# Kernel optimization log

Hardware: AMD Instinct MI355X
Metric: run time of the kernel (lower is better)

Reference implementation:

```python
import jax, jax.numpy as jnp
import numpy as np
from jax.scipy.special import digamma, gammaln

NUM_CLASSES = 3
FOCAL_GAMMA = 2.0
LABEL_SMOOTHING = 0.1
EVIDENTIAL_W = 0.1
CONTRASTIVE_W = 0.1
BOUNDARY_W = 0.15
TRIPLET_W = 0.1
QUALITY_W = 0.1
TRIPLET_MARGIN = 1.5


def setup_inputs() -> dict:
    key = jax.random.key(0)
    k1, k2, k3 = jax.random.split(key, 3)
    B, D = 4096, 512
    logits = jax.random.normal(k1, (B, NUM_CLASSES), dtype=jnp.float32)
    targets = jax.random.randint(k2, (B,), 0, 3)
    features = jax.random.normal(k3, (B, D), dtype=jnp.float32)
    alpha = jax.random.uniform(jax.random.fold_in(key, 7), (B, NUM_CLASSES), dtype=jnp.float32)
    focal_alpha = jnp.array([1.0, 2.0, 1.5], dtype=jnp.float32)
    class_weights = jnp.array([1.0, 2.0, 1.5], dtype=jnp.float32)
    return {"logits": logits, "targets": targets, "features": features,
            "alpha": alpha, "epoch": 1, "focal_alpha": focal_alpha,
            "class_weights": class_weights}


def reference(logits, targets, features, alpha, epoch, focal_alpha, class_weights):
    B = logits.shape[0]
    C = NUM_CLASSES

    # ---- focal loss (label-smoothed CE, torch semantics) ----
    logp = jax.nn.log_softmax(logits, axis=1)                      # [B,C]
    nll = -jnp.take_along_axis(logp, targets[:, None], axis=1)[:, 0]
    ce_ls = (1.0 - LABEL_SMOOTHING) * nll + LABEL_SMOOTHING * (-logp.mean(axis=1))
    pt = jnp.exp(-ce_ls)
    focal = (focal_alpha[targets] * (1.0 - pt) ** FOCAL_GAMMA * ce_ls).mean()

    # ---- weighted CE (torch weighted mean: sum(w*nll)/sum(w)) ----
    w = class_weights[targets]
    ce = (w * nll).sum() / w.sum()

    # ---- enhanced boundary loss ----
    probs = jax.nn.softmax(logits, axis=1)
    real = targets == 0
    semi = targets == 1
    syn = targets == 2
    rb = jnp.where(real, probs[:, 1] + 0.6 * probs[:, 2], 0.0).sum()
    sb = jnp.where(syn, probs[:, 1] + 0.4 * probs[:, 0], 0.0).sum()
    mb = jnp.where(semi, 1.0 - probs[:, 1] + 0.3 * (probs[:, 0] + probs[:, 2]), 0.0).sum()
    boundary = (rb + sb + 4.5 * mb) / (B + 1e-8)

    total = 0.4 * focal + 0.3 * ce + BOUNDARY_W * boundary

    # ---- normalized features and pairwise cosine-sim matrix ----
    norms = jnp.linalg.norm(features, axis=1, keepdims=True)
    f = features / jnp.maximum(norms, 1e-12)
    sim = f @ f.T                                                  # [B,B]
    same = targets[:, None] == targets[None, :]
    eye = jnp.eye(B, dtype=bool)

    # ---- enhanced contrastive loss ----
    pos = jnp.where(same, (1.0 - sim) ** 2, 0.0).sum()
    neg = jnp.where(~same, jnp.clip(sim - 0.2, 0.0) ** 2, 0.0).sum()
    semi_pair = semi[:, None] & semi[None, :]
    semi_l = jnp.where(semi_pair, (1.0 - sim) ** 2, 0.0).sum()
    contrastive = (pos + neg + 4.0 * semi_l) / (B * B + 1e-8)

    # ---- enhanced triplet loss (batch-hard, vectorized) ----
    d2 = jnp.clip(2.0 - 2.0 * sim, 0.0)
    dist = jnp.sqrt(jnp.where(eye, 1.0, d2))  # diag masked; safe sqrt
    pos_mask = same & ~eye
    neg_mask = ~same
    hp = jnp.max(jnp.where(pos_mask, dist, -jnp.inf), axis=1)
    hn = jnp.min(jnp.where(neg_mask, dist, jnp.inf), axis=1)
    valid = pos_mask.any(axis=1) & neg_mask.any(axis=1)
    margin = TRIPLET_MARGIN * jnp.where(targets == 1, 2.5, 1.0)
    tl = jax.nn.relu(hp - hn + margin)
    cnt = valid.sum()
    triplet = jnp.where(cnt > 0,
                        jnp.where(valid, tl, 0.0).sum() / jnp.maximum(cnt, 1),
                        0.0)

    # ---- quality-invariant loss (upper-tri same-class pairs) ----
    upper = jnp.triu(jnp.ones((B, B), dtype=bool), k=1)
    qmask = same & upper
    npairs = qmask.sum()
    q = jnp.where(qmask, (1.0 - sim) ** 2, 0.0).sum() / jnp.maximum(npairs, 1)
    frac2 = syn.astype(jnp.float32).mean()
    q = q * jnp.where(syn.sum() > 0, 1.0 + 2.5 * frac2, 1.0)
    quality = jnp.where(npairs > 0, q, 0.0)

    # ---- evidential loss ----
    onehot = jax.nn.one_hot(targets, C, dtype=jnp.float32)
    S = alpha.sum(axis=1, keepdims=True) + 1e-8
    likelihood = (onehot * (digamma(S) - digamma(alpha + 1e-8))).sum(axis=1)
    at = onehot + (1.0 - onehot) * alpha
    ats = at.sum(axis=1) + 1e-8
    kl = (gammaln(ats) - gammaln(at + 1e-8).sum(axis=1)
          + ((at - 1.0) * (digamma(at + 1e-8) - digamma(ats[:, None] + 1e-8))).sum(axis=1))
    annealing = min(1.0, (epoch / 25.0) ** 2)
    evidential = likelihood.mean() + annealing * 0.2 * kl.mean()

    total = (total + CONTRASTIVE_W * contrastive + TRIPLET_W * triplet
             + QUALITY_W * quality + EVIDENTIAL_W * evidential)
    return total
```

## Files before the change

kernel.cpp:

```cpp
#include <hip/hip_runtime.h>
#include <hip/hip_bf16.h>
#include <cstdint>

typedef __attribute__((ext_vector_type(8))) __bf16 bf8;
typedef __attribute__((ext_vector_type(4))) float f32x4;

#if defined(__has_builtin)
#if __has_builtin(__builtin_amdgcn_global_load_lds)
#define USE_GLL 1
#endif
#endif
#ifndef USE_GLL
#define USE_GLL 0
#endif

#if USE_GLL
__device__ __forceinline__ void gll16(const __bf16* g, __bf16* l){
  __builtin_amdgcn_global_load_lds(
      (const __attribute__((address_space(1))) void*)g,
      (__attribute__((address_space(3))) void*)l, 16, 0, 0);
}
#endif

__device__ __forceinline__ unsigned mapf(float x){
  unsigned u = __float_as_uint(x);
  return (u & 0x80000000u) ? ~u : (u | 0x80000000u);
}
__device__ __forceinline__ float unmapf(unsigned u){
  return __uint_as_float((u & 0x80000000u) ? (u & 0x7FFFFFFFu) : ~u);
}

__device__ float digammaf_(float x){
  float r = 0.f;
  while (x < 6.f){ r -= 1.f/x; x += 1.f; }
  float inv = 1.f/x, inv2 = inv*inv;
  r += logf(x) - 0.5f*inv
     - inv2*(0.08333333333f - inv2*(0.008333333333f - inv2*0.003968253968f));
  return r;
}

__global__ __launch_bounds__(256) void k_prep(const float* __restrict__ feat,
    __bf16* __restrict__ fb,
    const float* __restrict__ logits, const int* __restrict__ targets,
    const float* __restrict__ alpha,  const float* __restrict__ fa,
    const float* __restrict__ cw, int B, int D,
    float* __restrict__ psum, unsigned* __restrict__ pcnt,
    float* __restrict__ acc, unsigned* rowMinU, unsigned* rowMaxU){
  int bid = blockIdx.x, tid = threadIdx.x;
  int wave = tid >> 6, lane = tid & 63;

  int row = bid*4 + wave;
  if (row < B){
    const float* src = feat + (size_t)row*D;
    float ss = 0.f;
    for (int c = lane*4; c < D; c += 64*4){
      float4 v = *(const float4*)(src + c);
      ss += v.x*v.x + v.y*v.y + v.z*v.z + v.w*v.w;
    }
    #pragma unroll
    for (int off=32; off; off>>=1) ss += __shfl_xor(ss, off);
    float inv = 1.f / fmaxf(sqrtf(ss), 1e-12f);
    __bf16* dst = fb + (size_t)row*D;
    for (int c = lane*8; c < D; c += 64*8){
      float4 v0 = *(const float4*)(src + c);
      float4 v1 = *(const float4*)(src + c + 4);
      bf8 o;
      o[0]=(__bf16)(v0.x*inv); o[1]=(__bf16)(v0.y*inv);
      o[2]=(__bf16)(v0.z*inv); o[3]=(__bf16)(v0.w*inv);
      o[4]=(__bf16)(v1.x*inv); o[5]=(__bf16)(v1.y*inv);
      o[6]=(__bf16)(v1.z*inv); o[7]=(__bf16)(v1.w*inv);
      *(bf8*)(dst + c) = o;
    }
  }

  int SB = B >> 8;
  if (bid == SB && tid < 16) acc[tid] = 0.f;
  if (bid >= SB) return;

  int i = bid*256 + tid;
  rowMinU[i] = 0xFFFFFFFFu; rowMaxU[i] = 0u;

  float l0=logits[3*i], l1=logits[3*i+1], l2=logits[3*i+2];
  int t = targets[i];
  float m = fmaxf(l0, fmaxf(l1,l2));
  float e0=expf(l0-m), e1=expf(l1-m), e2=expf(l2-m);
  float se = e0+e1+e2;
  float lse = m + logf(se);
  float lp0=l0-lse, lp1=l1-lse, lp2=l2-lse;
  float lpt = (t==0)?lp0:((t==1)?lp1:lp2);
  float nll = -lpt;
  float ce_ls = 0.9f*nll + 0.1f*(-(lp0+lp1+lp2)*(1.f/3.f));
  float pt = expf(-ce_ls);
  float om = 1.f - pt;
  float focal_i = fa[t]*om*om*ce_ls;
  float w = cw[t];
  float ce_n = w*nll, ce_d = w;
  float p0=e0/se, p1=e1/se, p2=e2/se;
  float bnd;
  if (t==0)      bnd = p1 + 0.6f*p2;
  else if (t==2) bnd = p1 + 0.4f*p0;
  else           bnd = 4.5f*(1.f - p1 + 0.3f*(p0+p2));
  float a0=alpha[3*i], a1=alpha[3*i+1], a2=alpha[3*i+2];
  float S = a0+a1+a2 + 1e-8f;
  float at_ = (t==0)?a0:((t==1)?a1:a2);
  float lik = digammaf_(S) - digammaf_(at_ + 1e-8f);
  float b0 = (t==0)?1.f:a0, b1 = (t==1)?1.f:a1, b2 = (t==2)?1.f:a2;
  float ats = b0+b1+b2 + 1e-8f;
  float psa = digammaf_(ats + 1e-8f);
  float kl = lgammaf(ats)
     - (lgammaf(b0+1e-8f)+lgammaf(b1+1e-8f)+lgammaf(b2+1e-8f))
     + (b0-1.f)*(digammaf_(b0+1e-8f)-psa)
     + (b1-1.f)*(digammaf_(b1+1e-8f)-psa)
     + (b2-1.f)*(digammaf_(b2+1e-8f)-psa);

  unsigned long long m0 = __ballot(t==0);
  unsigned long long m1 = __ballot(t==1);
  unsigned long long m2 = __ballot(t==2);
  #pragma unroll
  for (int off=32; off; off>>=1){
    focal_i += __shfl_xor(focal_i, off);
    ce_n    += __shfl_xor(ce_n, off);
    ce_d    += __shfl_xor(ce_d, off);
    bnd     += __shfl_xor(bnd, off);
    lik     += __shfl_xor(lik, off);
    kl      += __shfl_xor(kl, off);
  }
  if (lane == 0){
    int slot = bid*4 + wave;
    psum[slot*8+0]=focal_i; psum[slot*8+1]=ce_n; psum[slot*8+2]=ce_d;
    psum[slot*8+3]=bnd;     psum[slot*8+4]=lik;  psum[slot*8+5]=kl;
    pcnt[slot*4+0]=(unsigned)__popcll(m0);
    pcnt[slot*4+1]=(unsigned)__popcll(m1);
    pcnt[slot*4+2]=(unsigned)__popcll(m2);
  }
}

__global__ __launch_bounds__(256) void k_pairs(const __bf16* __restrict__ fb,
    const int* __restrict__ targets, int B, int D,
    float* acc, unsigned* rowMinU, unsigned* rowMaxU){
  __shared__ __bf16 sA[2][4096];
  __shared__ __bf16 sB[2][4096];
  __shared__ int sRT[128];
  __shared__ int sCT[128];
  __shared__ float sred[4][4];

  int t = blockIdx.x;
  int bx = (int)((sqrtf(8.f*(float)t + 1.f) - 1.f)*0.5f);
  while ((bx+1)*(bx+2)/2 <= t) bx++;
  while (bx*(bx+1)/2 > t) bx--;
  int by = t - bx*(bx+1)/2;
  bool isDiag = (by == bx);
  int rowBase = by*128, colBase = bx*128;

  int tid = threadIdx.x, lane = tid & 63, wave = tid >> 6;
  int wr = wave >> 1, wc = wave & 1;
  int quad = lane >> 4, l16 = lane & 15;

  if (tid < 128) sRT[tid] = targets[rowBase + tid];
  else           sCT[tid-128] = targets[colBase + tid - 128];

  const __bf16* gA[2]; const __bf16* gB[2];
  #pragma unroll
  for (int r=0; r<2; r++){
    int e = tid*8 + r*2048;
    int row = e >> 5;
    int cb = (e & 31) >> 3;
    int gcb = cb ^ ((row >> 1) & 3);
    gA[r] = fb + (size_t)(rowBase + row)*D + gcb*8;
    gB[r] = fb + (size_t)(colBase + row)*D + gcb*8;
  }
  int wofs = wave*512;

  int offA[4], offB[4];
  #pragma unroll
  for (int mi=0; mi<4; mi++){
    int R = wr*64 + mi*16 + l16;
    offA[mi] = R*32 + ((quad ^ ((R>>1)&3))*8);
  }
  #pragma unroll
  for (int ni=0; ni<4; ni++){
    int R = wc*64 + ni*16 + l16;
    offB[ni] = R*32 + ((quad ^ ((R>>1)&3))*8);
  }

#if USE_GLL
  #pragma unroll
  for (int r=0; r<2; r++){
    gll16(gA[r], &sA[0][wofs + r*2048]);
    gll16(gB[r], &sB[0][wofs + r*2048]);
  }
#else
  #pragma unroll
  for (int r=0; r<2; r++){
    *(bf8*)&sA[0][tid*8 + r*2048] = *(const bf8*)gA[r];
    *(bf8*)&sB[0][tid*8 + r*2048] = *(const bf8*)gB[r];
  }
#endif

  f32x4 C[4][4] = {};
  int NIT = D/32;
  int cur = 0;

  for (int it=0; it<NIT; ++it){
    __syncthreads();
    if (it+1 < NIT){
      int k0 = (it+1)*32;
      int nb = cur ^ 1;
#if USE_GLL
      #pragma unroll
      for (int r=0; r<2; r++){
        gll16(gA[r]+k0, &sA[nb][wofs + r*2048]);
        gll16(gB[r]+k0, &sB[nb][wofs + r*2048]);
      }
#else
      #pragma unroll
      for (int r=0; r<2; r++){
        *(bf8*)&sA[nb][tid*8 + r*2048] = *(const bf8*)(gA[r]+k0);
        *(bf8*)&sB[nb][tid*8 + r*2048] = *(const bf8*)(gB[r]+k0);
      }
#endif
    }
    bf8 aF[4], bF[4];
    #pragma unroll
    for (int mi=0; mi<4; mi++) aF[mi] = *(const bf8*)(&sA[cur][offA[mi]]);
    #pragma unroll
    for (int ni=0; ni<4; ni++) bF[ni] = *(const bf8*)(&sB[cur][offB[ni]]);
    #pragma unroll
    for (int mi=0; mi<4; mi++)
      #pragma unroll
      for (int ni=0; ni<4; ni++)
        C[mi][ni] = __builtin_amdgcn_mfma_f32_16x16x32_bf16(aF[mi], bF[ni], C[mi][ni], 0,0,0);
    cur ^= 1;
  }

  int tcol[4];
  #pragma unroll
  for (int ni=0; ni<4; ni++) tcol[ni] = sCT[wc*64 + ni*16 + l16];

  float pos=0.f, neg=0.f, semi=0.f, diag=0.f;
  float cmin[4], cmax[4];
  #pragma unroll
  for (int ni=0; ni<4; ni++){ cmin[ni]=2.f; cmax[ni]=-2.f; }

  #pragma unroll
  for (int mi=0; mi<4; mi++){
    #pragma unroll
    for (int r=0; r<4; r++){
      int rl = wr*64 + mi*16 + quad*4 + r;
      int row = rowBase + rl;
      int tr = sRT[rl];
      float vmin = 2.f, vmax = -2.f;
      #pragma unroll
      for (int ni=0; ni<4; ni++){
        int col = colBase + wc*64 + ni*16 + l16;
        float s = C[mi][ni][r];
        if (tr == tcol[ni]){
          float omv = 1.f - s;
          float q = omv*omv;
          pos += q;
          if (tr == 1) semi += q;
          if (row == col) diag += q;
          else {
            vmin = fminf(vmin, s);
            cmin[ni] = fminf(cmin[ni], s);
          }
        } else {
          float c0 = fmaxf(s - 0.2f, 0.f);
          neg += c0*c0;
          vmax = fmaxf(vmax, s);
          cmax[ni] = fmaxf(cmax[ni], s);
        }
      }
      #pragma unroll
      for (int off=1; off<16; off<<=1){
        vmin = fminf(vmin, __shfl_xor(vmin, off));
        vmax = fmaxf(vmax, __shfl_xor(vmax, off));
      }
      if (l16 == 0){
        atomicMin(&rowMinU[row], mapf(vmin));
        atomicMax(&rowMaxU[row], mapf(vmax));
      }
    }
  }

  if (!isDiag){
    #pragma unroll
    for (int ni=0; ni<4; ni++){
      float cn = cmin[ni], cx = cmax[ni];
      cn = fminf(cn, __shfl_xor(cn, 16)); cn = fminf(cn, __shfl_xor(cn, 32));
      cx = fmaxf(cx, __shfl_xor(cx, 16)); cx = fmaxf(cx, __shfl_xor(cx, 32));
      if (quad == 0){
        int col = colBase + wc*64 + ni*16 + l16;
        atomicMin(&rowMinU[col], mapf(cn));
        atomicMax(&rowMaxU[col], mapf(cx));
      }
    }
  }

  #pragma unroll
  for (int off=32; off; off>>=1){
    pos  += __shfl_xor(pos, off);
    neg  += __shfl_xor(neg, off);
    semi += __shfl_xor(semi, off);
    diag += __shfl_xor(diag, off);
  }
  if (lane == 0){ sred[wave][0]=pos; sred[wave][1]=neg; sred[wave][2]=semi; sred[wave][3]=diag; }
  __syncthreads();
  if (tid == 0){
    float fac = isDiag ? 1.f : 2.f;
    float p=0,n=0,s2=0,d=0;
    for (int w2=0; w2<4; w2++){ p+=sred[w2][0]; n+=sred[w2][1]; s2+=sred[w2][2]; d+=sred[w2][3]; }
    atomicAdd(&acc[0], p*fac); atomicAdd(&acc[1], n*fac);
    atomicAdd(&acc[2], s2*fac); atomicAdd(&acc[3], d);
  }
}

__global__ __launch_bounds__(256) void k_final(const int* __restrict__ targets,
    const int* __restrict__ epoch_p, int B, int SB,
    const float* acc, const float* psum, const unsigned* pcnt,
    const unsigned* rowMinU, const unsigned* rowMaxU, float* out){
  __shared__ float tot[6];
  __shared__ unsigned cn[3];
  int tid = threadIdx.x;
  int nslots = SB*4;

  if (tid < 64){
    float v0=0,v1=0,v2=0,v3=0,v4=0,v5=0;
    int c0=0,c1=0,c2=0;
    for (int s=tid; s<nslots; s+=64){
      v0+=psum[s*8+0]; v1+=psum[s*8+1]; v2+=psum[s*8+2];
      v3+=psum[s*8+3]; v4+=psum[s*8+4]; v5+=psum[s*8+5];
      c0+=(int)pcnt[s*4+0]; c1+=(int)pcnt[s*4+1]; c2+=(int)pcnt[s*4+2];
    }
    #pragma unroll
    for (int off=32; off; off>>=1){
      v0+=__shfl_xor(v0,off); v1+=__shfl_xor(v1,off); v2+=__shfl_xor(v2,off);
      v3+=__shfl_xor(v3,off); v4+=__shfl_xor(v4,off); v5+=__shfl_xor(v5,off);
      c0+=__shfl_xor(c0,off); c1+=__shfl_xor(c1,off); c2+=__shfl_xor(c2,off);
    }
    if (tid == 0){
      tot[0]=v0; tot[1]=v1; tot[2]=v2; tot[3]=v3; tot[4]=v4; tot[5]=v5;
      cn[0]=(unsigned)c0; cn[1]=(unsigned)c1; cn[2]=(unsigned)c2;
    }
  }
  __syncthreads();
  int n0=(int)cn[0], n1=(int)cn[1], n2=(int)cn[2];

  float tsum = 0.f, tcnt = 0.f;
  for (int i = tid; i < B; i += 256){
    int t = targets[i];
    int nt = (t==0)?n0:((t==1)?n1:n2);
    if (nt - 1 > 0 && B - nt > 0){
      float mn = unmapf(rowMinU[i]);
      float mx = unmapf(rowMaxU[i]);
      float hp = sqrtf(fmaxf(2.f - 2.f*mn, 0.f));
      float hn = sqrtf(fmaxf(2.f - 2.f*mx, 0.f));
      float margin = 1.5f * ((t==1) ? 2.5f : 1.f);
      float tl = fmaxf(hp - hn + margin, 0.f);
      tsum += tl; tcnt += 1.f;
    }
  }
  #pragma unroll
  for (int off=32; off; off>>=1){ tsum += __shfl_xor(tsum, off); tcnt += __shfl_xor(tcnt, off); }
  __shared__ float sb[4][2];
  int wave = tid>>6, lane = tid&63;
  if (lane==0){ sb[wave][0]=tsum; sb[wave][1]=tcnt; }
  __syncthreads();
  if (tid==0){
    float ts=0, tn=0;
    for (int w2=0;w2<4;w2++){ ts+=sb[w2][0]; tn+=sb[w2][1]; }
    float triplet = (tn > 0.f) ? ts / fmaxf(tn, 1.f) : 0.f;
    float pos=acc[0], neg=acc[1], semi=acc[2], diag=acc[3];
    float Bf = (float)B;
    float focal = tot[0] / Bf;
    float ce = tot[1] / tot[2];
    float boundary = tot[3] / (Bf + 1e-8f);
    float contrastive = (pos + neg + 4.f*semi) / (Bf*Bf + 1e-8f);
    long long npl = ((long long)n0*(n0-1) + (long long)n1*(n1-1) + (long long)n2*(n2-1))/2;
    float qsum = (pos - diag) * 0.5f;
    float q = qsum / (float)(npl > 0 ? npl : 1);
    if (n2 > 0) q *= (1.f + 2.5f * ((float)n2 / Bf));
    float quality = (npl > 0) ? q : 0.f;
    int ep = epoch_p[0];
    float er = (float)ep / 25.f;
    float ann = fminf(1.f, er*er);
    float evidential = tot[4]/Bf + ann*0.2f*tot[5]/Bf;
    float total = 0.4f*focal + 0.3f*ce + 0.15f*boundary
                + 0.1f*contrastive + 0.1f*triplet + 0.1f*quality + 0.1f*evidential;
    out[0] = total;
  }
}

extern "C" void kernel_launch(void* const* d_in, const int* in_sizes, int n_in,
                              void* d_out, int out_size, void* d_ws, size_t ws_size,
                              hipStream_t stream){
  const float* logits   = (const float*)d_in[0];
  const int*   targets  = (const int*)d_in[1];
  const float* features = (const float*)d_in[2];
  const float* alpha    = (const float*)d_in[3];
  const int*   epoch    = (const int*)d_in[4];
  const float* fa       = (const float*)d_in[5];
  const float* cw       = (const float*)d_in[6];
  int B = in_sizes[1];
  int D = in_sizes[2] / B;
  int SB = B >> 8;

  char* ws = (char*)d_ws;
  float*    acc     = (float*)ws;
  unsigned* pcnt    = (unsigned*)(ws + 128);
  float*    psum    = (float*)(ws + 128 + (size_t)SB*64);
  unsigned* rowMinU = (unsigned*)(ws + 4096);
  unsigned* rowMaxU = (unsigned*)(ws + 4096 + (size_t)B*4);
  __bf16*   fb      = (__bf16*)(ws + 4096 + (size_t)B*8);

  k_prep <<<B/4, 256, 0, stream>>>(features, fb, logits, targets, alpha, fa, cw,
                                   B, D, psum, pcnt, acc, rowMinU, rowMaxU);
  int ntile = B/128;
  int nblk  = ntile*(ntile+1)/2;
  k_pairs<<<nblk, 256, 0, stream>>>(fb, targets, B, D, acc, rowMinU, rowMaxU);
  k_final<<<1, 256, 0, stream>>>(targets, epoch, B, SB, acc, psum, pcnt,
                                 rowMinU, rowMaxU, (float*)d_out);
}
```

Before: 138.1 us.

## Shrink pairwise sim tiles to 64x64 and replace float atomics with per-block partials

The Gram-matrix kernel now uses 64x64 output tiles instead of 128x128, with a 2x2 MFMA fragment per wave, smaller LDS buffers, a launch-bounds occupancy hint, and a manually unrolled double-buffer loop. This launches roughly four times as many blocks (2080 vs 528), to fill the GPU's compute units and raise occupancy. Global float atomics for the pair accumulators are replaced by per-block partial writes reduced in the final kernel. The trade-off is lower operand reuse per block, more global loads of the features, and more min/max atomics on the row arrays.

```diff
diff --git a/kernel.cpp b/kernel.cpp
--- a/kernel.cpp
+++ b/kernel.cpp
@@ -45,7 +45,7 @@
     const float* __restrict__ alpha,  const float* __restrict__ fa,
     const float* __restrict__ cw, int B, int D,
     float* __restrict__ psum, unsigned* __restrict__ pcnt,
-    float* __restrict__ acc, unsigned* rowMinU, unsigned* rowMaxU){
+    unsigned* rowMinU, unsigned* rowMaxU){
   int bid = blockIdx.x, tid = threadIdx.x;
   int wave = tid >> 6, lane = tid & 63;
 
@@ -74,7 +74,6 @@
   }
 
   int SB = B >> 8;
-  if (bid == SB && tid < 16) acc[tid] = 0.f;
   if (bid >= SB) return;
 
   int i = bid*256 + tid;
@@ -135,13 +134,13 @@
   }
 }
 
-__global__ __launch_bounds__(256) void k_pairs(const __bf16* __restrict__ fb,
+__global__ __launch_bounds__(256, 6) void k_pairs(const __bf16* __restrict__ fb,
     const int* __restrict__ targets, int B, int D,
-    float* acc, unsigned* rowMinU, unsigned* rowMaxU){
-  __shared__ __bf16 sA[2][4096];
-  __shared__ __bf16 sB[2][4096];
-  __shared__ int sRT[128];
-  __shared__ int sCT[128];
+    float* __restrict__ pairPart, unsigned* rowMinU, unsigned* rowMaxU){
+  __shared__ __bf16 sA[2][2048];
+  __shared__ __bf16 sB[2][2048];
+  __shared__ int sRT[64];
+  __shared__ int sCT[64];
   __shared__ float sred[4][4];
 
   int t = blockIdx.x;
@@ -150,109 +149,86 @@
   while (bx*(bx+1)/2 > t) bx--;
   int by = t - bx*(bx+1)/2;
   bool isDiag = (by == bx);
-  int rowBase = by*128, colBase = bx*128;
+  int rowBase = by*64, colBase = bx*64;
 
   int tid = threadIdx.x, lane = tid & 63, wave = tid >> 6;
   int wr = wave >> 1, wc = wave & 1;
   int quad = lane >> 4, l16 = lane & 15;
 
-  if (tid < 128) sRT[tid] = targets[rowBase + tid];
-  else           sCT[tid-128] = targets[colBase + tid - 128];
-
-  const __bf16* gA[2]; const __bf16* gB[2];
-  #pragma unroll
-  for (int r=0; r<2; r++){
-    int e = tid*8 + r*2048;
-    int row = e >> 5;
-    int cb = (e & 31) >> 3;
-    int gcb = cb ^ ((row >> 1) & 3);
-    gA[r] = fb + (size_t)(rowBase + row)*D + gcb*8;
-    gB[r] = fb + (size_t)(colBase + row)*D + gcb*8;
-  }
+  if (tid < 64)       sRT[tid] = targets[rowBase + tid];
+  else if (tid < 128) sCT[tid-64] = targets[colBase + tid - 64];
+
+  int srow = tid >> 2;
+  int scb  = (tid & 3) ^ ((srow >> 1) & 3);
+  const __bf16* gA = fb + (size_t)(rowBase + srow)*D + scb*8;
+  const __bf16* gB = fb + (size_t)(colBase + srow)*D + scb*8;
   int wofs = wave*512;
 
-  int offA[4], offB[4];
-  #pragma unroll
-  for (int mi=0; mi<4; mi++){
-    int R = wr*64 + mi*16 + l16;
+  int offA[2], offB[2];
+  #pragma unroll
+  for (int mi=0; mi<2; mi++){
+    int R = wr*32 + mi*16 + l16;
     offA[mi] = R*32 + ((quad ^ ((R>>1)&3))*8);
   }
   #pragma unroll
-  for (int ni=0; ni<4; ni++){
-    int R = wc*64 + ni*16 + l16;
+  for (int ni=0; ni<2; ni++){
+    int R = wc*32 + ni*16 + l16;
     offB[ni] = R*32 + ((quad ^ ((R>>1)&3))*8);
   }
 
+  f32x4 C[2][2] = {};
+  int NIT = D/32;
+
 #if USE_GLL
-  #pragma unroll
-  for (int r=0; r<2; r++){
-    gll16(gA[r], &sA[0][wofs + r*2048]);
-    gll16(gB[r], &sB[0][wofs + r*2048]);
-  }
+  #define STAGE(buf, k0) do{ gll16(gA + (k0), &sA[buf][wofs]); \
+                             gll16(gB + (k0), &sB[buf][wofs]); }while(0)
 #else
-  #pragma unroll
-  for (int r=0; r<2; r++){
-    *(bf8*)&sA[0][tid*8 + r*2048] = *(const bf8*)gA[r];
-    *(bf8*)&sB[0][tid*8 + r*2048] = *(const bf8*)gB[r];
-  }
+  #define STAGE(buf, k0) do{ *(bf8*)&sA[buf][tid*8] = *(const bf8*)(gA + (k0)); \
+                             *(bf8*)&sB[buf][tid*8] = *(const bf8*)(gB + (k0)); }while(0)
 #endif
 
-  f32x4 C[4][4] = {};
-  int NIT = D/32;
-  int cur = 0;
-
-  for (int it=0; it<NIT; ++it){
+  STAGE(0, 0);
+
+  #define COMPUTE(buf) do{ \
+    bf8 aF0 = *(const bf8*)(&sA[buf][offA[0]]); \
+    bf8 aF1 = *(const bf8*)(&sA[buf][offA[1]]); \
+    bf8 bF0 = *(const bf8*)(&sB[buf][offB[0]]); \
+    bf8 bF1 = *(const bf8*)(&sB[buf][offB[1]]); \
+    C[0][0] = __builtin_amdgcn_mfma_f32_16x16x32_bf16(aF0, bF0, C[0][0], 0,0,0); \
+    C[0][1] = __builtin_amdgcn_mfma_f32_16x16x32_bf16(aF0, bF1, C[0][1], 0,0,0); \
+    C[1][0] = __builtin_amdgcn_mfma_f32_16x16x32_bf16(aF1, bF0, C[1][0], 0,0,0); \
+    C[1][1] = __builtin_amdgcn_mfma_f32_16x16x32_bf16(aF1, bF1, C[1][1], 0,0,0); \
+  }while(0)
+
+  for (int it=0; it<NIT; it+=2){
     __syncthreads();
-    if (it+1 < NIT){
-      int k0 = (it+1)*32;
-      int nb = cur ^ 1;
-#if USE_GLL
-      #pragma unroll
-      for (int r=0; r<2; r++){
-        gll16(gA[r]+k0, &sA[nb][wofs + r*2048]);
-        gll16(gB[r]+k0, &sB[nb][wofs + r*2048]);
-      }
-#else
-      #pragma unroll
-      for (int r=0; r<2; r++){
-        *(bf8*)&sA[nb][tid*8 + r*2048] = *(const bf8*)(gA[r]+k0);
-        *(bf8*)&sB[nb][tid*8 + r*2048] = *(const bf8*)(gB[r]+k0);
-      }
-#endif
-    }
-    bf8 aF[4], bF[4];
-    #pragma unroll
-    for (int mi=0; mi<4; mi++) aF[mi] = *(const bf8*)(&sA[cur][offA[mi]]);
-    #pragma unroll
-    for (int ni=0; ni<4; ni++) bF[ni] = *(const bf8*)(&sB[cur][offB[ni]]);
-    #pragma unroll
-    for (int mi=0; mi<4; mi++)
-      #pragma unroll
-      for (int ni=0; ni<4; ni++)
-        C[mi][ni] = __builtin_amdgcn_mfma_f32_16x16x32_bf16(aF[mi], bF[ni], C[mi][ni], 0,0,0);
-    cur ^= 1;
-  }
-
-  int tcol[4];
-  #pragma unroll
-  for (int ni=0; ni<4; ni++) tcol[ni] = sCT[wc*64 + ni*16 + l16];
+    STAGE(1, (it+1)*32);
+    COMPUTE(0);
+    __syncthreads();
+    if (it+2 < NIT) STAGE(0, (it+2)*32);
+    COMPUTE(1);
+  }
+
+  int tcol[2];
+  #pragma unroll
+  for (int ni=0; ni<2; ni++) tcol[ni] = sCT[wc*32 + ni*16 + l16];
 
   float pos=0.f, neg=0.f, semi=0.f, diag=0.f;
-  float cmin[4], cmax[4];
-  #pragma unroll
-  for (int ni=0; ni<4; ni++){ cmin[ni]=2.f; cmax[ni]=-2.f; }
-
-  #pragma unroll
-  for (int mi=0; mi<4; mi++){
+  float cmin[2], cmax[2];
+  #pragma unroll
+  for (int ni=0; ni<2; ni++){ cmin[ni]=2.f; cmax[ni]=-2.f; }
+
+  #pragma unroll
+  for (int mi=0; mi<2; mi++){
     #pragma unroll
     for (int r=0; r<4; r++){
-      int rl = wr*64 + mi*16 + quad*4 + r;
+      int rl = wr*32 + mi*16 + quad*4 + r;
       int row = rowBase + rl;
       int tr = sRT[rl];
       float vmin = 2.f, vmax = -2.f;
       #pragma unroll
-      for (int ni=0; ni<4; ni++){
-        int col = colBase + wc*64 + ni*16 + l16;
+      for (int ni=0; ni<2; ni++){
+        int col = colBase + wc*32 + ni*16 + l16;
         float s = C[mi][ni][r];
         if (tr == tcol[ni]){
           float omv = 1.f - s;
@@ -285,12 +261,12 @@
 
   if (!isDiag){
     #pragma unroll
-    for (int ni=0; ni<4; ni++){
+    for (int ni=0; ni<2; ni++){
       float cn = cmin[ni], cx = cmax[ni];
       cn = fminf(cn, __shfl_xor(cn, 16)); cn = fminf(cn, __shfl_xor(cn, 32));
       cx = fmaxf(cx, __shfl_xor(cx, 16)); cx = fmaxf(cx, __shfl_xor(cx, 32));
       if (quad == 0){
-        int col = colBase + wc*64 + ni*16 + l16;
+        int col = colBase + wc*32 + ni*16 + l16;
         atomicMin(&rowMinU[col], mapf(cn));
         atomicMax(&rowMaxU[col], mapf(cx));
       }
@@ -310,19 +286,24 @@
     float fac = isDiag ? 1.f : 2.f;
     float p=0,n=0,s2=0,d=0;
     for (int w2=0; w2<4; w2++){ p+=sred[w2][0]; n+=sred[w2][1]; s2+=sred[w2][2]; d+=sred[w2][3]; }
-    atomicAdd(&acc[0], p*fac); atomicAdd(&acc[1], n*fac);
-    atomicAdd(&acc[2], s2*fac); atomicAdd(&acc[3], d);
+    pairPart[blockIdx.x*4+0] = p*fac;
+    pairPart[blockIdx.x*4+1] = n*fac;
+    pairPart[blockIdx.x*4+2] = s2*fac;
+    pairPart[blockIdx.x*4+3] = d;
   }
 }
 
 __global__ __launch_bounds__(256) void k_final(const int* __restrict__ targets,
-    const int* __restrict__ epoch_p, int B, int SB,
-    const float* acc, const float* psum, const unsigned* pcnt,
+    const int* __restrict__ epoch_p, int B, int SB, int nblk,
+    const float* __restrict__ pairPart, const float* __restrict__ psum,
+    const unsigned* __restrict__ pcnt,
     const unsigned* rowMinU, const unsigned* rowMaxU, float* out){
   __shared__ float tot[6];
   __shared__ unsigned cn[3];
+  __shared__ float ptot[4];
   int tid = threadIdx.x;
   int nslots = SB*4;
+  int wave = tid>>6, lane = tid&63;
 
   if (tid < 64){
     float v0=0,v1=0,v2=0,v3=0,v4=0,v5=0;
@@ -341,6 +322,27 @@
     if (tid == 0){
       tot[0]=v0; tot[1]=v1; tot[2]=v2; tot[3]=v3; tot[4]=v4; tot[5]=v5;
       cn[0]=(unsigned)c0; cn[1]=(unsigned)c1; cn[2]=(unsigned)c2;
+    }
+  }
+
+  {
+    float p=0,n=0,s2=0,d=0;
+    for (int s=tid; s<nblk; s+=256){
+      p += pairPart[s*4+0]; n += pairPart[s*4+1];
+      s2+= pairPart[s*4+2]; d += pairPart[s*4+3];
+    }
+    #pragma unroll
+    for (int off=32; off; off>>=1){
+      p+=__shfl_xor(p,off); n+=__shfl_xor(n,off);
+      s2+=__shfl_xor(s2,off); d+=__shfl_xor(d,off);
+    }
+    __shared__ float pw[4][4];
+    if (lane==0){ pw[wave][0]=p; pw[wave][1]=n; pw[wave][2]=s2; pw[wave][3]=d; }
+    __syncthreads();
+    if (tid==0){
+      float a=0,b=0,c=0,e=0;
+      for (int w2=0; w2<4; w2++){ a+=pw[w2][0]; b+=pw[w2][1]; c+=pw[w2][2]; e+=pw[w2][3]; }
+      ptot[0]=a; ptot[1]=b; ptot[2]=c; ptot[3]=e;
     }
   }
   __syncthreads();
@@ -363,14 +365,13 @@
   #pragma unroll
   for (int off=32; off; off>>=1){ tsum += __shfl_xor(tsum, off); tcnt += __shfl_xor(tcnt, off); }
   __shared__ float sb[4][2];
-  int wave = tid>>6, lane = tid&63;
   if (lane==0){ sb[wave][0]=tsum; sb[wave][1]=tcnt; }
   __syncthreads();
   if (tid==0){
     float ts=0, tn=0;
     for (int w2=0;w2<4;w2++){ ts+=sb[w2][0]; tn+=sb[w2][1]; }
     float triplet = (tn > 0.f) ? ts / fmaxf(tn, 1.f) : 0.f;
-    float pos=acc[0], neg=acc[1], semi=acc[2], diag=acc[3];
+    float pos=ptot[0], neg=ptot[1], semi=ptot[2], diag=ptot[3];
     float Bf = (float)B;
     float focal = tot[0] / Bf;
     float ce = tot[1] / tot[2];
@@ -404,20 +405,20 @@
   int B = in_sizes[1];
   int D = in_sizes[2] / B;
   int SB = B >> 8;
+  int T  = B / 64;
+  int nblk = T*(T+1)/2;
 
   char* ws = (char*)d_ws;
-  float*    acc     = (float*)ws;
-  unsigned* pcnt    = (unsigned*)(ws + 128);
-  float*    psum    = (float*)(ws + 128 + (size_t)SB*64);
-  unsigned* rowMinU = (unsigned*)(ws + 4096);
-  unsigned* rowMaxU = (unsigned*)(ws + 4096 + (size_t)B*4);
-  __bf16*   fb      = (__bf16*)(ws + 4096 + (size_t)B*8);
+  unsigned* pcnt     = (unsigned*)(ws);
+  float*    psum     = (float*)(ws + 16384);
+  float*    pairPart = (float*)(ws + 32768);
+  unsigned* rowMinU  = (unsigned*)(ws + 131072);
+  unsigned* rowMaxU  = (unsigned*)(ws + 131072 + (size_t)B*4);
+  __bf16*   fb       = (__bf16*)(ws + 131072 + (size_t)B*8);
 
   k_prep <<<B/4, 256, 0, stream>>>(features, fb, logits, targets, alpha, fa, cw,
-                                   B, D, psum, pcnt, acc, rowMinU, rowMaxU);
-  int ntile = B/128;
-  int nblk  = ntile*(ntile+1)/2;
-  k_pairs<<<nblk, 256, 0, stream>>>(fb, targets, B, D, acc, rowMinU, rowMaxU);
-  k_final<<<1, 256, 0, stream>>>(targets, epoch, B, SB, acc, psum, pcnt,
+                                   B, D, psum, pcnt, rowMinU, rowMaxU);
+  k_pairs<<<nblk, 256, 0, stream>>>(fb, targets, B, D, pairPart, rowMinU, rowMaxU);
+  k_final<<<1, 256, 0, stream>>>(targets, epoch, B, SB, nblk, pairPart, psum, pcnt,
                                  rowMinU, rowMaxU, (float*)d_out);
 }
```

Measured after the change: 129.4 us. 1.07x faster.
